# Optimization experiments

Measured on AMD Instinct MI355X. Metric: run time of the kernel, lower is better.

Reference implementation:

```python
import jax, jax.numpy as jnp
import numpy as np

N_TOKENS = 8192
HIDDEN = 4096
N_EXPERTS = 64
TOP_K = 8


def setup_inputs() -> dict:
    key = jax.random.key(0)
    k1, k2 = jax.random.split(key)
    h = jax.random.normal(k1, (N_TOKENS, HIDDEN), dtype=jnp.float32)
    weight = jax.random.normal(k2, (N_EXPERTS, HIDDEN), dtype=jnp.float32) * (1.0 / np.sqrt(HIDDEN))
    return {"h": h, "weight": weight}


def reference(h, weight):
    # logits = h @ W^T in fp32  -> [n_tokens, n_experts]
    logits = jnp.einsum("th,eh->te", h.astype(jnp.float32), weight.astype(jnp.float32))
    scores = jax.nn.softmax(logits, axis=-1)
    topk_weight, topk_idx = jax.lax.top_k(scores, TOP_K)  # [n_tokens, k]
    return topk_weight, topk_idx
```

## Files before the change

kernel.cpp:

```cpp
#include <hip/hip_runtime.h>
#include <math.h>
#include <stdint.h>

#define NTOK 8192
#define HID  4096
#define NEXP 64
#define TOPK 8

typedef float    f32x4 __attribute__((ext_vector_type(4)));
typedef _Float16 f16x8 __attribute__((ext_vector_type(8)));


__device__ __forceinline__ void cvt_hilo(f32x4 a, f32x4 b, f16x8& hi, f16x8& lo)
{
    float x[8] = {a.x, a.y, a.z, a.w, b.x, b.y, b.z, b.w};
#pragma unroll
    for (int j = 0; j < 8; ++j) {
        const _Float16 h = (_Float16)x[j];
        hi[j] = h;
        lo[j] = (_Float16)(x[j] - (float)h);
    }
}

__device__ __forceinline__ void gll16(const void* g, void* l) {
    __builtin_amdgcn_global_load_lds(
        (const __attribute__((address_space(1))) uint32_t*)g,
        (__attribute__((address_space(3))) uint32_t*)l, 16, 0, 0);
}

#define MFMA16(AH, BH, AC) \
    AC = __builtin_amdgcn_mfma_f32_16x16x32_f16(AH, BH, AC, 0, 0, 0)

__global__ __launch_bounds__(256)
void k0_pack(const float* __restrict__ W, f16x8* __restrict__ wq)
{
    const int gidx = blockIdx.x * 256 + threadIdx.x;
    const int s = gidx >> 8;
    const int E = (gidx >> 6) & 3;
    const int l = gidx & 63;
    const int e = E * 16 + (l & 15);
    const int k = s * 32 + ((l >> 4) << 3);

    const float* src = W + (size_t)e * HID + k;
    const f32x4 w0 = *(const f32x4*)src;
    const f32x4 w1 = *(const f32x4*)(src + 4);
    f16x8 hi, lo;
    cvt_hilo(w0 * 2048.0f, w1 * 2048.0f, hi, lo);

    wq[s * 512 + E * 128 + l]      = hi;
    wq[s * 512 + E * 128 + 64 + l] = lo;
}

#define STAGE_A(S) \
    gll16(hap + (size_t)(S) * 128,  &LDSB[((S) % 5) * 8192 + tid * 16])
#define STAGE_B(S) \
    gll16(bap + (size_t)(S) * 8192, &LDSB[40960 + ((S) % 4) * 8192 + tid * 16])

#define KSTEP(S, VN) do {                                                     \
    if ((S) + 2 < 32) STAGE_B((S) + 2);                                       \
    if ((S) + 3 < 32) STAGE_A((S) + 3);                                       \
    asm volatile("s_waitcnt vmcnt(" #VN ")" ::: "memory");                    \
    __builtin_amdgcn_sched_barrier(0);                                        \
    __builtin_amdgcn_s_barrier();                                             \
    __builtin_amdgcn_sched_barrier(0);                                        \
    const char* _A = &LDSB[((S) % 5) * 8192];                                 \
    const char* _B = &LDSB[40960 + ((S) % 4) * 8192];                         \
    const f32x4 a0 = *(const f32x4*)&_A[ga0 * 16];                            \
    const f32x4 a1 = *(const f32x4*)&_A[ga1 * 16];                            \
    const f16x8 bh0 = *(const f16x8*)&_B[(E0 * 128 + l) * 16];                \
    const f16x8 bl0 = *(const f16x8*)&_B[(E0 * 128 + 64 + l) * 16];           \
    const f16x8 bh1 = *(const f16x8*)&_B[(E1 * 128 + l) * 16];                \
    const f16x8 bl1 = *(const f16x8*)&_B[(E1 * 128 + 64 + l) * 16];           \
    f16x8 _ah, _al; cvt_hilo(a0, a1, _ah, _al);                               \
    MFMA16(_ah, bh0, acH0); MFMA16(_ah, bh1, acH1);                           \
    MFMA16(_ah, bl0, acC0); MFMA16(_ah, bl1, acC1);                           \
    MFMA16(_al, bh0, acC0); MFMA16(_al, bh1, acC1);                           \
} while (0)

__global__ __launch_bounds__(512, 2)
void k1_logits(const float* __restrict__ Hm, const char* __restrict__ wqc,
               float* __restrict__ lgp)
{
    __shared__ char LDSB[73728];

    const int tid  = threadIdx.x;
    const int wave = tid >> 6;
    const int l    = tid & 63;
    const int kg   = l >> 4;
    const int tg   = wave >> 1;
    const int eg   = wave & 1;
    const int E0   = eg * 2;
    const int E1   = eg * 2 + 1;
    const int tokg = blockIdx.x >> 2;
    const int ksb  = blockIdx.x & 3;
    const int tok0 = tokg * 64;
    const int kb   = ksb * 1024;

    const int tloc = tg * 16 + (l & 15);
    const int ga0  = tloc * 8 + ((kg * 2)     ^ (l & 7));
    const int ga1  = tloc * 8 + ((kg * 2 + 1) ^ (l & 7));

    const int st = tid >> 3;
    const int so = tid & 7;
    const char* hap = (const char*)(Hm + (size_t)(tok0 + st) * HID + kb)
                    + ((so ^ (st & 7)) * 16);
    const char* bap = wqc + (size_t)ksb * 262144 + tid * 16;

    f32x4 acH0 = (f32x4)(0.f), acH1 = (f32x4)(0.f);
    f32x4 acC0 = (f32x4)(0.f), acC1 = (f32x4)(0.f);

    STAGE_A(0); STAGE_B(0); STAGE_A(1); STAGE_B(1); STAGE_A(2);

    KSTEP( 0, 5); KSTEP( 1, 5); KSTEP( 2, 5); KSTEP( 3, 5);
    KSTEP( 4, 5); KSTEP( 5, 5); KSTEP( 6, 5); KSTEP( 7, 5);
    KSTEP( 8, 5); KSTEP( 9, 5); KSTEP(10, 5); KSTEP(11, 5);
    KSTEP(12, 5); KSTEP(13, 5); KSTEP(14, 5); KSTEP(15, 5);
    KSTEP(16, 5); KSTEP(17, 5); KSTEP(18, 5); KSTEP(19, 5);
    KSTEP(20, 5); KSTEP(21, 5); KSTEP(22, 5); KSTEP(23, 5);
    KSTEP(24, 5); KSTEP(25, 5); KSTEP(26, 5); KSTEP(27, 5);
    KSTEP(28, 5); KSTEP(29, 4); KSTEP(30, 2); KSTEP(31, 0);

    const f32x4 v0 = acH0 + acC0;
    const f32x4 v1 = acH1 + acC1;
    float* o = lgp + ((size_t)ksb * NTOK + tok0 + tg * 16) * 64 + eg * 32;
#pragma unroll
    for (int r = 0; r < 4; ++r) {
        const int row = (kg << 2) + r;
        o[row * 64 +      (l & 15)] = v0[r];
        o[row * 64 + 16 + (l & 15)] = v1[r];
    }
}

__global__ __launch_bounds__(256)
void k2_finish(const float* __restrict__ lgp, float* __restrict__ out)
{
    __shared__ __align__(16) float sc[4][64];
    const int tid  = threadIdx.x;
    const int wave = tid >> 6;
    const int lane = tid & 63;
    float* outw = out;
    float* outi = out + (size_t)NTOK * TOPK;

    const int tok = blockIdx.x * 4 + wave;
    const float* p = lgp + (size_t)tok * 64 + lane;
    const size_t SL = (size_t)NTOK * 64;
    const float lgv = ((p[0] + p[SL]) + (p[2 * SL] + p[3 * SL])) * (1.0f / 2048.0f);

    float mx = lgv;
#pragma unroll
    for (int off = 32; off; off >>= 1) mx = fmaxf(mx, __shfl_xor(mx, off));
    const float pv = expf(lgv - mx);
    float ss = pv;
#pragma unroll
    for (int off = 32; off; off >>= 1) ss += __shfl_xor(ss, off);
    ss = __shfl(ss, 0);
    const float sval = pv / ss;

    sc[wave][lane] = sval;
    __syncthreads();

    int rank = 0;
#pragma unroll
    for (int j4 = 0; j4 < 16; ++j4) {
        const f32x4 v = *(const f32x4*)&sc[wave][j4 * 4];
#pragma unroll
        for (int u = 0; u < 4; ++u) {
            const int j = j4 * 4 + u;
            rank += (v[u] > sval || (v[u] == sval && j < lane)) ? 1 : 0;
        }
    }
    if (rank < TOPK) {
        outw[(size_t)tok * TOPK + rank] = sval;
        outi[(size_t)tok * TOPK + rank] = (float)lane;
    }
}

extern "C" void kernel_launch(void* const* d_in, const int* in_sizes, int n_in,
                              void* d_out, int out_size, void* d_ws, size_t ws_size,
                              hipStream_t stream) {
    (void)in_sizes; (void)n_in; (void)out_size; (void)ws_size;
    const float* h = (const float*)d_in[0];
    const float* w = (const float*)d_in[1];
    float* out = (float*)d_out;

    f16x8* wq  = (f16x8*)d_ws;
    float* lgp = (float*)((char*)d_ws + (1 << 20));

    k0_pack<<<128, 256, 0, stream>>>(w, wq);
    k1_logits<<<512, 512, 0, stream>>>(h, (const char*)wq, lgp);
    k2_finish<<<NTOK / 4, 256, 0, stream>>>(lgp, out);
}
```

Baseline: 39.59 us.

## Halve logits block to 256 threads with 2x per-wave token tile

Shrinks the logits kernel block from 512 to 256 threads, and each wave now covers 32 tokens instead of 16 with two A fragments and eight accumulators. Each thread issues two async global-to-LDS loads per stage, and the wait counts are doubled to match. Each B fragment read from LDS is now reused across two A fragments, cutting LDS reads and barrier participants per MFMA. The cost is more registers per thread and fewer waves to hide memory latency.

```diff
diff --git a/kernel.cpp b/kernel.cpp
--- a/kernel.cpp
+++ b/kernel.cpp
@@ -51,10 +51,14 @@
     wq[s * 512 + E * 128 + 64 + l] = lo;
 }
 
-#define STAGE_A(S) \
-    gll16(hap + (size_t)(S) * 128,  &LDSB[((S) % 5) * 8192 + tid * 16])
-#define STAGE_B(S) \
-    gll16(bap + (size_t)(S) * 8192, &LDSB[40960 + ((S) % 4) * 8192 + tid * 16])
+#define STAGE_A(S) do {                                                       \
+    gll16(hap0 + (size_t)(S) * 128, &LDSB[((S) % 5) * 8192 + tid * 16]);      \
+    gll16(hap1 + (size_t)(S) * 128, &LDSB[((S) % 5) * 8192 + 4096 + tid * 16]); \
+} while (0)
+#define STAGE_B(S) do {                                                       \
+    gll16(bap + (size_t)(S) * 8192,        &LDSB[40960 + ((S) % 4) * 8192 + tid * 16]); \
+    gll16(bap + (size_t)(S) * 8192 + 4096, &LDSB[40960 + ((S) % 4) * 8192 + 4096 + tid * 16]); \
+} while (0)
 
 #define KSTEP(S, VN) do {                                                     \
     if ((S) + 2 < 32) STAGE_B((S) + 2);                                       \
@@ -65,19 +69,26 @@
     __builtin_amdgcn_sched_barrier(0);                                        \
     const char* _A = &LDSB[((S) % 5) * 8192];                                 \
     const char* _B = &LDSB[40960 + ((S) % 4) * 8192];                         \
-    const f32x4 a0 = *(const f32x4*)&_A[ga0 * 16];                            \
-    const f32x4 a1 = *(const f32x4*)&_A[ga1 * 16];                            \
+    const f32x4 a00 = *(const f32x4*)&_A[ga00 * 16];                          \
+    const f32x4 a01 = *(const f32x4*)&_A[ga01 * 16];                          \
+    const f32x4 a10 = *(const f32x4*)&_A[ga10 * 16];                          \
+    const f32x4 a11 = *(const f32x4*)&_A[ga11 * 16];                          \
     const f16x8 bh0 = *(const f16x8*)&_B[(E0 * 128 + l) * 16];                \
     const f16x8 bl0 = *(const f16x8*)&_B[(E0 * 128 + 64 + l) * 16];           \
     const f16x8 bh1 = *(const f16x8*)&_B[(E1 * 128 + l) * 16];                \
     const f16x8 bl1 = *(const f16x8*)&_B[(E1 * 128 + 64 + l) * 16];           \
-    f16x8 _ah, _al; cvt_hilo(a0, a1, _ah, _al);                               \
-    MFMA16(_ah, bh0, acH0); MFMA16(_ah, bh1, acH1);                           \
-    MFMA16(_ah, bl0, acC0); MFMA16(_ah, bl1, acC1);                           \
-    MFMA16(_al, bh0, acC0); MFMA16(_al, bh1, acC1);                           \
+    f16x8 ah0, al0, ah1, al1;                                                 \
+    cvt_hilo(a00, a01, ah0, al0);                                             \
+    cvt_hilo(a10, a11, ah1, al1);                                             \
+    MFMA16(ah0, bh0, acH00); MFMA16(ah0, bh1, acH01);                         \
+    MFMA16(ah1, bh0, acH10); MFMA16(ah1, bh1, acH11);                         \
+    MFMA16(ah0, bl0, acC00); MFMA16(ah0, bl1, acC01);                         \
+    MFMA16(ah1, bl0, acC10); MFMA16(ah1, bl1, acC11);                         \
+    MFMA16(al0, bh0, acC00); MFMA16(al0, bh1, acC01);                         \
+    MFMA16(al1, bh0, acC10); MFMA16(al1, bh1, acC11);                         \
 } while (0)
 
-__global__ __launch_bounds__(512, 2)
+__global__ __launch_bounds__(256, 2)
 void k1_logits(const float* __restrict__ Hm, const char* __restrict__ wqc,
                float* __restrict__ lgp)
 {
@@ -96,38 +107,47 @@
     const int tok0 = tokg * 64;
     const int kb   = ksb * 1024;
 
-    const int tloc = tg * 16 + (l & 15);
-    const int ga0  = tloc * 8 + ((kg * 2)     ^ (l & 7));
-    const int ga1  = tloc * 8 + ((kg * 2 + 1) ^ (l & 7));
+    const int tl0  = tg * 32 + (l & 15);
+    const int tl1  = tl0 + 16;
+    const int ga00 = tl0 * 8 + ((kg * 2)     ^ (l & 7));
+    const int ga01 = tl0 * 8 + ((kg * 2 + 1) ^ (l & 7));
+    const int ga10 = tl1 * 8 + ((kg * 2)     ^ (l & 7));
+    const int ga11 = tl1 * 8 + ((kg * 2 + 1) ^ (l & 7));
 
     const int st = tid >> 3;
     const int so = tid & 7;
-    const char* hap = (const char*)(Hm + (size_t)(tok0 + st) * HID + kb)
-                    + ((so ^ (st & 7)) * 16);
-    const char* bap = wqc + (size_t)ksb * 262144 + tid * 16;
-
-    f32x4 acH0 = (f32x4)(0.f), acH1 = (f32x4)(0.f);
-    f32x4 acC0 = (f32x4)(0.f), acC1 = (f32x4)(0.f);
+    const char* hap0 = (const char*)(Hm + (size_t)(tok0 + st) * HID + kb)
+                     + ((so ^ (st & 7)) * 16);
+    const char* hap1 = (const char*)(Hm + (size_t)(tok0 + 32 + st) * HID + kb)
+                     + ((so ^ (st & 7)) * 16);
+    const char* bap  = wqc + (size_t)ksb * 262144 + tid * 16;
+
+    f32x4 acH00 = (f32x4)(0.f), acH01 = (f32x4)(0.f);
+    f32x4 acH10 = (f32x4)(0.f), acH11 = (f32x4)(0.f);
+    f32x4 acC00 = (f32x4)(0.f), acC01 = (f32x4)(0.f);
+    f32x4 acC10 = (f32x4)(0.f), acC11 = (f32x4)(0.f);
 
     STAGE_A(0); STAGE_B(0); STAGE_A(1); STAGE_B(1); STAGE_A(2);
 
-    KSTEP( 0, 5); KSTEP( 1, 5); KSTEP( 2, 5); KSTEP( 3, 5);
-    KSTEP( 4, 5); KSTEP( 5, 5); KSTEP( 6, 5); KSTEP( 7, 5);
-    KSTEP( 8, 5); KSTEP( 9, 5); KSTEP(10, 5); KSTEP(11, 5);
-    KSTEP(12, 5); KSTEP(13, 5); KSTEP(14, 5); KSTEP(15, 5);
-    KSTEP(16, 5); KSTEP(17, 5); KSTEP(18, 5); KSTEP(19, 5);
-    KSTEP(20, 5); KSTEP(21, 5); KSTEP(22, 5); KSTEP(23, 5);
-    KSTEP(24, 5); KSTEP(25, 5); KSTEP(26, 5); KSTEP(27, 5);
-    KSTEP(28, 5); KSTEP(29, 4); KSTEP(30, 2); KSTEP(31, 0);
-
-    const f32x4 v0 = acH0 + acC0;
-    const f32x4 v1 = acH1 + acC1;
-    float* o = lgp + ((size_t)ksb * NTOK + tok0 + tg * 16) * 64 + eg * 32;
+    KSTEP( 0, 10); KSTEP( 1, 10); KSTEP( 2, 10); KSTEP( 3, 10);
+    KSTEP( 4, 10); KSTEP( 5, 10); KSTEP( 6, 10); KSTEP( 7, 10);
+    KSTEP( 8, 10); KSTEP( 9, 10); KSTEP(10, 10); KSTEP(11, 10);
+    KSTEP(12, 10); KSTEP(13, 10); KSTEP(14, 10); KSTEP(15, 10);
+    KSTEP(16, 10); KSTEP(17, 10); KSTEP(18, 10); KSTEP(19, 10);
+    KSTEP(20, 10); KSTEP(21, 10); KSTEP(22, 10); KSTEP(23, 10);
+    KSTEP(24, 10); KSTEP(25, 10); KSTEP(26, 10); KSTEP(27, 10);
+    KSTEP(28, 10); KSTEP(29,  8); KSTEP(30,  4); KSTEP(31,  0);
+
+    const f32x4 v00 = acH00 + acC00, v01 = acH01 + acC01;
+    const f32x4 v10 = acH10 + acC10, v11 = acH11 + acC11;
+    float* o = lgp + ((size_t)ksb * NTOK + tok0 + tg * 32) * 64 + eg * 32;
 #pragma unroll
     for (int r = 0; r < 4; ++r) {
         const int row = (kg << 2) + r;
-        o[row * 64 +      (l & 15)] = v0[r];
-        o[row * 64 + 16 + (l & 15)] = v1[r];
+        o[row * 64 +            (l & 15)] = v00[r];
+        o[row * 64 +       16 + (l & 15)] = v01[r];
+        o[(row + 16) * 64 +     (l & 15)] = v10[r];
+        o[(row + 16) * 64 + 16 + (l & 15)] = v11[r];
     }
 }
 
@@ -187,6 +207,6 @@
     float* lgp = (float*)((char*)d_ws + (1 << 20));
 
     k0_pack<<<128, 256, 0, stream>>>(w, wq);
-    k1_logits<<<512, 512, 0, stream>>>(h, (const char*)wq, lgp);
+    k1_logits<<<512, 256, 0, stream>>>(h, (const char*)wq, lgp);
     k2_finish<<<NTOK / 4, 256, 0, stream>>>(lgp, out);
 }
```

Measured after the change: 39.76 us. About the same (+0.4%).
